# Kernel optimization log

Hardware: AMD Instinct MI355X
Metric: run time of the kernel (lower is better)

Reference implementation:

```python
import jax, jax.numpy as jnp
import numpy as np

B, C, H, W = 32, 512, 32, 32
N = H * W            # seq_len = 1024
HEADS = 8
DH = C // HEADS      # 64
K = 256              # linformer low-rank
EPS = 1e-5


def setup_inputs() -> dict:
    key = jax.random.key(0)
    ks = jax.random.split(key, 10)
    s = 0.02
    return {
        "x": jax.random.normal(ks[0], (B, C, H, W), dtype=jnp.float32),
        "pos": jax.random.normal(ks[1], (1, N, C), dtype=jnp.float32),
        "ln_g": jnp.ones((C,), dtype=jnp.float32),
        "ln_b": jnp.zeros((C,), dtype=jnp.float32),
        "Wq": jax.random.normal(ks[2], (C, C), dtype=jnp.float32) * s,
        "Wk": jax.random.normal(ks[3], (C, C), dtype=jnp.float32) * s,
        "Wv": jax.random.normal(ks[4], (C, C), dtype=jnp.float32) * s,
        "proj_k": jax.random.normal(ks[5], (N, K), dtype=jnp.float32) * s,
        "proj_v": jax.random.normal(ks[6], (N, K), dtype=jnp.float32) * s,
        "Wo": jax.random.normal(ks[7], (C, C), dtype=jnp.float32) * s,
        "bo": jnp.zeros((C,), dtype=jnp.float32),
    }


def reference(x, pos, ln_g, ln_b, Wq, Wk, Wv, proj_k, proj_v, Wo, bo):
    b, c, h, w = x.shape
    n = h * w
    # b c h w -> b (h w) c
    xf = x.reshape(b, c, n).transpose(0, 2, 1) + pos
    # LayerNorm (biased variance, eps=1e-5) + ReLU; dropout = identity (eval)
    mu = xf.mean(-1, keepdims=True)
    var = jnp.var(xf, axis=-1, keepdims=True)
    y = (xf - mu) * jax.lax.rsqrt(var + EPS) * ln_g + ln_b
    y = jax.nn.relu(y)
    # Linformer self-attention
    q = y @ Wq                                   # [b,n,c]
    k_ = jnp.einsum('bnd,nk->bkd', y @ Wk, proj_k)  # [b,K,c]
    v_ = jnp.einsum('bnd,nk->bkd', y @ Wv, proj_v)  # [b,K,c]
    q = q.reshape(b, n, HEADS, DH)
    k_ = k_.reshape(b, K, HEADS, DH)
    v_ = v_.reshape(b, K, HEADS, DH)
    dots = jnp.einsum('bnhd,bkhd->bhnk', q, k_) * (DH ** -0.5)
    attn = jax.nn.softmax(dots, axis=-1)
    out = jnp.einsum('bhnk,bkhd->bnhd', attn, v_).reshape(b, n, c)
    out = out @ Wo + bo
    # residual with (x + pos), then back to b c h w
    out = out + xf
    return out.transpose(0, 2, 1).reshape(b, c, h, w)
```

## Files before the change

### kernel.cpp

```cpp
#include <hip/hip_runtime.h>
#include <hip/hip_bf16.h>
#include <cstdint>

#define BB  32
#define CC  512
#define NN  1024
#define HH  8
#define DHH 64
#define KR  256

using f32x4  = __attribute__((ext_vector_type(4))) float;
using f32x16 = __attribute__((ext_vector_type(16))) float;
using bf16x8 = __attribute__((ext_vector_type(8))) __bf16;
using u32x4  = __attribute__((ext_vector_type(4))) unsigned int;

__device__ __forceinline__ unsigned short f2bf(float f) {
  unsigned int u = __float_as_uint(f);
  u += 0x7fffu + ((u >> 16) & 1u);
  return (unsigned short)(u >> 16);
}

__device__ __forceinline__ unsigned int pknat(float a, float b) {
  unsigned short ua = __builtin_bit_cast(unsigned short, (__bf16)a);
  unsigned short ub = __builtin_bit_cast(unsigned short, (__bf16)b);
  return (unsigned int)ua | ((unsigned int)ub << 16);
}

__device__ __forceinline__ void gload16(const void* gsrc, void* ldst) {
  __builtin_amdgcn_global_load_lds(
      (const __attribute__((address_space(1))) unsigned int*)gsrc,
      (__attribute__((address_space(3))) unsigned int*)ldst, 16, 0, 0);
}

__global__ __launch_bounds__(256) void transcvt_all(
    const float* __restrict__ w0, const float* __restrict__ w1,
    const float* __restrict__ w2, const float* __restrict__ w3,
    const float* __restrict__ p0, const float* __restrict__ p1,
    unsigned short* __restrict__ d0, unsigned short* __restrict__ d1,
    unsigned short* __restrict__ d2, unsigned short* __restrict__ d3,
    unsigned short* __restrict__ e0, unsigned short* __restrict__ e1) {
  const int m = blockIdx.y;
  const float* src = m==0?w0:m==1?w1:m==2?w2:m==3?w3:m==4?p0:p1;
  unsigned short* dst = m==0?d0:m==1?d1:m==2?d2:m==3?d3:m==4?e0:e1;
  const int R = (m < 4) ? 512 : 1024;
  const int logC = (m < 4) ? 9 : 8;
  int idx = blockIdx.x * 256 + threadIdx.x;
  int r = idx >> logC, c = idx & ((1 << logC) - 1);
  dst[(size_t)c * R + r] = f2bf(src[idx]);
}

__global__ __launch_bounds__(256) void posT_kernel(
    const float* __restrict__ pos, float* __restrict__ posT) {
  int idx = blockIdx.x * 256 + threadIdx.x;
  int c = idx >> 10, n = idx & 1023;
  posT[idx] = pos[(size_t)n * CC + c];
}

__global__ __launch_bounds__(256) void ln_relu_kernel(
    const float* __restrict__ x, const float* __restrict__ pos,
    const float* __restrict__ g, const float* __restrict__ bta,
    unsigned short* __restrict__ y, unsigned short* __restrict__ yT) {
  __shared__ float tile[16][528];
  __shared__ float smu[16], srs[16];
  const int b = blockIdx.y, n0 = blockIdx.x * 16;
  const int tid = threadIdx.x;
  const float* xb = x + (size_t)b * CC * NN;

  {
    const int q4 = (tid & 3) * 4;
    #pragma unroll
    for (int p = 0; p < 8; ++p) {
      int c = p * 64 + (tid >> 2);
      float4 v = *reinterpret_cast<const float4*>(&xb[(size_t)c * NN + n0 + q4]);
      tile[q4 + 0][c] = v.x;
      tile[q4 + 1][c] = v.y;
      tile[q4 + 2][c] = v.z;
      tile[q4 + 3][c] = v.w;
    }
  }
  __syncthreads();

  const int c4 = (tid & 127) * 4;
  #pragma unroll
  for (int p = 0; p < 8; ++p) {
    int nl = 2 * p + (tid >> 7);
    float4 pv = *reinterpret_cast<const float4*>(&pos[(size_t)(n0 + nl) * CC + c4]);
    float4* tp = reinterpret_cast<float4*>(&tile[nl][c4]);
    float4 t = *tp;
    t.x += pv.x; t.y += pv.y; t.z += pv.z; t.w += pv.w;
    *tp = t;
  }
  __syncthreads();

  {
    const int r = tid >> 4, l16 = tid & 15;
    float s = 0.f, s2 = 0.f;
    #pragma unroll
    for (int i = 0; i < 32; ++i) {
      float v = tile[r][l16 + i * 16];
      s += v; s2 += v * v;
    }
    #pragma unroll
    for (int d = 1; d < 16; d <<= 1) { s += __shfl_xor(s, d); s2 += __shfl_xor(s2, d); }
    if (l16 == 0) {
      float mu = s * (1.f / 512.f);
      float var = s2 * (1.f / 512.f) - mu * mu;
      smu[r] = mu;
      srs[r] = rsqrtf(var + 1e-5f);
    }
  }
  __syncthreads();

  unsigned short* yb = y + ((size_t)b * NN + n0) * CC;
  const float4 gv = *reinterpret_cast<const float4*>(&g[c4]);
  const float4 bv = *reinterpret_cast<const float4*>(&bta[c4]);
  #pragma unroll
  for (int p = 0; p < 8; ++p) {
    int nl = 2 * p + (tid >> 7);
    float mu = smu[nl], rs = srs[nl];
    float4* tp = reinterpret_cast<float4*>(&tile[nl][c4]);
    float4 t = *tp;
    float4 o;
    o.x = (t.x - mu) * rs * gv.x + bv.x; o.x = o.x > 0.f ? o.x : 0.f;
    o.y = (t.y - mu) * rs * gv.y + bv.y; o.y = o.y > 0.f ? o.y : 0.f;
    o.z = (t.z - mu) * rs * gv.z + bv.z; o.z = o.z > 0.f ? o.z : 0.f;
    o.w = (t.w - mu) * rs * gv.w + bv.w; o.w = o.w > 0.f ? o.w : 0.f;
    uint2 u; u.x = pknat(o.x, o.y); u.y = pknat(o.z, o.w);
    *reinterpret_cast<uint2*>(&yb[(size_t)nl * CC + c4]) = u;
    *tp = o;
  }
  __syncthreads();

  unsigned short* ytb = yT + (size_t)b * CC * NN + n0;
  #pragma unroll
  for (int h = 0; h < 2; ++h) {
    int cc = h * 256 + tid;
    unsigned int pk8[8];
    #pragma unroll
    for (int p = 0; p < 8; ++p)
      pk8[p] = pknat(tile[2 * p][cc], tile[2 * p + 1][cc]);
    *reinterpret_cast<uint4*>(&ytb[(size_t)cc * NN])     = *reinterpret_cast<uint4*>(&pk8[0]);
    *reinterpret_cast<uint4*>(&ytb[(size_t)cc * NN + 8]) = *reinterpret_cast<uint4*>(&pk8[4]);
  }
}

template <int MODE>
__global__ __launch_bounds__(256) void gemm_tn(
    const unsigned short* __restrict__ A, int lda, long long strideA,
    const unsigned short* __restrict__ Bt, int ldb, long long strideB,
    unsigned short* __restrict__ Cb, long long strideC,
    int Nn, int Kk, int TB,
    const float* __restrict__ xres, const float* __restrict__ posT,
    const float* __restrict__ bias, float* __restrict__ outF) {
  __shared__ __align__(16) unsigned short sh[17408];
  unsigned short* aL = sh;
  unsigned short* bL = sh + 8192;
  const int nb = blockIdx.x * 128, mb = blockIdx.y * 128, zb = blockIdx.z;
  A  += (size_t)strideA * zb;
  Bt += (size_t)strideB * zb;
  if (MODE == 0 || MODE == 1) Cb += (size_t)strideC * zb;
  const int tid  = threadIdx.x;
  const int lane = tid & 63;
  const int wave = tid >> 6;
  const int wm = (wave >> 1) * 64, wn = (wave & 1) * 64;
  const int sr  = lane >> 2;
  const int scw = lane & 3;
  f32x4 acc[4][4] = {};

  auto stage = [&](int buf, int k0) {
    #pragma unroll
    for (int i = 0; i < 2; ++i) {
      int rbase = wave * 32 + i * 16;
      int row = rbase + sr;
      int ca = scw ^ ((row ^ (row >> 2)) & 3);
      gload16(&A [(size_t)(mb + row) * lda + k0 + ca * 8], &aL[buf * 4096 + rbase * 32]);
      gload16(&Bt[(size_t)(nb + row) * ldb + k0 + ca * 8], &bL[buf * 4096 + rbase * 32]);
    }
  };

  const int nt = Kk >> 5;
  stage(0, 0);
  __syncthreads();

  for (int t = 0; t < nt; ++t) {
    const int buf = t & 1;
    if (t + 1 < nt) stage(buf ^ 1, (t + 1) << 5);

    bf16x8 af[4], bfv[4];
    const int kc = lane >> 4;
    #pragma unroll
    for (int i = 0; i < 4; ++i) {
      int ra = wm + i * 16 + (lane & 15);
      int rb = wn + i * 16 + (lane & 15);
      af[i]  = *reinterpret_cast<const bf16x8*>(&aL[buf * 4096 + ra * 32 + (kc ^ ((ra ^ (ra >> 2)) & 3)) * 8]);
      bfv[i] = *reinterpret_cast<const bf16x8*>(&bL[buf * 4096 + rb * 32 + (kc ^ ((rb ^ (rb >> 2)) & 3)) * 8]);
    }
    #pragma unroll
    for (int i = 0; i < 4; ++i)
      #pragma unroll
      for (int j = 0; j < 4; ++j)
        acc[i][j] = __builtin_amdgcn_mfma_f32_16x16x32_bf16(af[i], bfv[j], acc[i][j], 0, 0, 0);
    __syncthreads();
  }

  if (MODE == 2) {
    float* Ct = reinterpret_cast<float*>(sh);
    const int halfsel = wave >> 1;
    const int t0base = nb & 1023;
    const int bcell = nb >> 10;
    #pragma unroll
    for (int half = 0; half < 2; ++half) {
      __syncthreads();
      if (halfsel == half) {
        #pragma unroll
        for (int i = 0; i < 4; ++i) {
          int rloc = i * 16 + ((lane >> 4) << 2);
          #pragma unroll
          for (int j = 0; j < 4; ++j) {
            int cl = wn + j * 16 + (lane & 15);
            #pragma unroll
            for (int t = 0; t < 4; ++t)
              Ct[(rloc + t) * 132 + cl] = acc[i][j][t];
          }
        }
      }
      __syncthreads();
      #pragma unroll
      for (int p8 = 0; p8 < 8; ++p8) {
        int e = p8 * 256 + tid;
        int r = e >> 5, f4 = (e & 31) * 4;
        int c = mb + half * 64 + r;
        size_t base = ((size_t)bcell * CC + c) * NN + t0base + f4;
        float4 cv = *reinterpret_cast<const float4*>(&Ct[r * 132 + f4]);
        float4 xv = *reinterpret_cast<const float4*>(&xres[base]);
        float4 pv = *reinterpret_cast<const float4*>(&posT[(size_t)c * NN + t0base + f4]);
        float bc = bias[c];
        float4 ov;
        ov.x = cv.x + xv.x + pv.x + bc;
        ov.y = cv.y + xv.y + pv.y + bc;
        ov.z = cv.z + xv.z + pv.z + bc;
        ov.w = cv.w + xv.w + pv.w + bc;
        *reinterpret_cast<float4*>(&outF[base]) = ov;
      }
    }
  } else {
    auto Ct = (unsigned short (*)[136])sh;
    __syncthreads();
    #pragma unroll
    for (int i = 0; i < 4; ++i) {
      const int r0 = wm + i * 16 + ((lane >> 4) << 2);
      #pragma unroll
      for (int j = 0; j < 4; ++j) {
        const int cl = wn + j * 16 + (lane & 15);
        #pragma unroll
        for (int t = 0; t < 4; ++t) {
          if (MODE == 0) Ct[r0 + t][cl] = f2bf(acc[i][j][t]);
          else           Ct[cl][r0 + t] = f2bf(acc[i][j][t]);
        }
      }
    }
    __syncthreads();
    const int rr = tid >> 4, ch = tid & 15;
    #pragma unroll
    for (int it = 0; it < 8; ++it) {
      const int r = it * 16 + rr;
      uint4 v = *reinterpret_cast<const uint4*>(&Ct[r][ch * 8]);
      if (MODE == 0)
        *reinterpret_cast<uint4*>(&Cb[(size_t)(mb + r) * Nn + nb + ch * 8]) = v;
      else
        *reinterpret_cast<uint4*>(&Cb[(size_t)(nb + r) * TB + mb + ch * 8]) = v;
    }
  }
}

__global__ __launch_bounds__(256, 2) void attn_kernel(
    const unsigned short* __restrict__ q,
    const unsigned short* __restrict__ kB,
    const unsigned short* __restrict__ vT,
    unsigned short* __restrict__ O) {
  __shared__ __align__(16) unsigned short smem[32768];
  const int wgid = blockIdx.x;
  const int grp  = wgid & 255;
  const int tg   = wgid >> 8;
  const int h = grp & 7, b = grp >> 3;
  const int wave = threadIdx.x >> 6, lane = threadIdx.x & 63;
  const int t32 = lane & 31, g2 = lane >> 5;
  const int tokb = tg * 128 + wave * 32;

  const unsigned short* qp = q + ((size_t)(b * NN + tokb + t32)) * CC + h * DHH + g2 * 8;
  bf16x8 qf[4];
  #pragma unroll
  for (int st = 0; st < 4; ++st)
    qf[st] = *reinterpret_cast<const bf16x8*>(qp + (size_t)st * 16);

  {
    const unsigned short* kb = kB + ((size_t)b * KR) * CC + h * DHH;
    const int r0w = wave * 64;
    #pragma unroll
    for (int i = 0; i < 8; ++i) {
      int row = r0w + i * 8 + (lane >> 3);
      int sc  = (lane & 7) ^ (row & 7);
      gload16(kb + (size_t)row * CC + sc * 8, &smem[(r0w + i * 8) * 64]);
    }
    const unsigned short* vb = vT + ((size_t)b * CC + h * DHH) * KR;
    const int v0w = wave * 16;
    #pragma unroll
    for (int i = 0; i < 8; ++i) {
      int row = v0w + i * 2 + (lane >> 5);
      int sc  = (lane & 31) ^ (row & 7);
      gload16(vb + (size_t)row * KR + sc * 8, &smem[16384 + (v0w + i * 2) * 256]);
    }
  }
  __syncthreads();

  f32x16 s8[8] = {};
  #pragma unroll
  for (int t8 = 0; t8 < 8; ++t8) {
    const int row = t8 * 32 + t32;
    #pragma unroll
    for (int st = 0; st < 4; ++st) {
      int ch = (2 * st + g2) ^ (row & 7);
      bf16x8 kf = *reinterpret_cast<const bf16x8*>(&smem[row * 64 + ch * 8]);
      s8[t8] = __builtin_amdgcn_mfma_f32_32x32x16_bf16(kf, qf[st], s8[t8], 0, 0, 0);
    }
  }

  float m = -1e30f;
  #pragma unroll
  for (int t8 = 0; t8 < 8; ++t8)
    #pragma unroll
    for (int r = 0; r < 16; ++r) m = fmaxf(m, s8[t8][r]);
  m = fmaxf(m, __shfl_xor(m, 32));
  const float cexp = 0.125f * 1.44269504088896f;
  float ls = 0.f;
  #pragma unroll
  for (int t8 = 0; t8 < 8; ++t8)
    #pragma unroll
    for (int r = 0; r < 16; ++r) {
      float p = __builtin_amdgcn_exp2f((s8[t8][r] - m) * cexp);
      s8[t8][r] = p;
      ls += p;
    }
  ls += __shfl_xor(ls, 32);
  float rinv = __builtin_amdgcn_rcpf(ls);

  f32x16 o0 = {}, o1 = {};
  #pragma unroll
  for (int t8 = 0; t8 < 8; ++t8) {
    unsigned int pkd[8];
    #pragma unroll
    for (int qq = 0; qq < 4; ++qq) {
      pkd[qq * 2 + 0] = pknat(s8[t8][4 * qq + 0], s8[t8][4 * qq + 1]);
      pkd[qq * 2 + 1] = pknat(s8[t8][4 * qq + 2], s8[t8][4 * qq + 3]);
    }
    #pragma unroll
    for (int a = 0; a < 2; ++a) {
      const int ks = t8 * 2 + a;
      unsigned int xe0 = pkd[4 * a + 0], xe1 = pkd[4 * a + 1];
      unsigned int xo0 = pkd[4 * a + 2], xo1 = pkd[4 * a + 3];
      unsigned int d0 = g2 ? __shfl_xor(xo0, 32) : xe0;
      unsigned int d1 = g2 ? __shfl_xor(xo1, 32) : xe1;
      unsigned int d2 = g2 ? xo0 : __shfl_xor(xe0, 32);
      unsigned int d3 = g2 ? xo1 : __shfl_xor(xe1, 32);
      u32x4 pv_ = {d0, d1, d2, d3};
      bf16x8 pa = __builtin_bit_cast(bf16x8, pv_);
      #pragma unroll
      for (int dt = 0; dt < 2; ++dt) {
        int row = dt * 32 + t32;
        int ch = (2 * ks + g2) ^ (row & 7);
        bf16x8 bv = *reinterpret_cast<const bf16x8*>(&smem[16384 + row * 256 + ch * 8]);
        if (dt == 0) o0 = __builtin_amdgcn_mfma_f32_32x32x16_bf16(pa, bv, o0, 0, 0, 0);
        else         o1 = __builtin_amdgcn_mfma_f32_32x32x16_bf16(pa, bv, o1, 0, 0, 0);
      }
    }
  }

  unsigned short* Ob = O + ((size_t)(b * NN + tokb)) * CC + h * DHH;
  #pragma unroll
  for (int r = 0; r < 16; ++r) {
    int tl = (r & 3) + 8 * (r >> 2) + 4 * g2;
    float rs = __shfl(rinv, tl);
    Ob[(size_t)tl * CC + t32]      = f2bf(o0[r] * rs);
    Ob[(size_t)tl * CC + 32 + t32] = f2bf(o1[r] * rs);
  }
}

extern "C" void kernel_launch(void* const* d_in, const int* in_sizes, int n_in,
                              void* d_out, int out_size, void* d_ws, size_t ws_size,
                              hipStream_t stream) {
  const float* x    = (const float*)d_in[0];
  const float* pos  = (const float*)d_in[1];
  const float* ln_g = (const float*)d_in[2];
  const float* ln_b = (const float*)d_in[3];
  const float* Wq   = (const float*)d_in[4];
  const float* Wk   = (const float*)d_in[5];
  const float* Wv   = (const float*)d_in[6];
  const float* pk   = (const float*)d_in[7];
  const float* pv   = (const float*)d_in[8];
  const float* Wo   = (const float*)d_in[9];
  const float* bo   = (const float*)d_in[10];
  float* out = (float*)d_out;

  unsigned short* ws = (unsigned short*)d_ws;
  size_t off = 0;
  auto alloc = [&](size_t elems) { unsigned short* p = ws + off; off += elems; return p; };
  unsigned short* WqT     = alloc(512 * 512);
  unsigned short* WkT     = alloc(512 * 512);
  unsigned short* WvT     = alloc(512 * 512);
  unsigned short* WoT     = alloc(512 * 512);
  unsigned short* projcat = alloc((size_t)512 * 1024);
  float*          posTb   = (float*)alloc((size_t)512 * 1024 * 2);
  unsigned short* yB      = alloc((size_t)32768 * 512);
  unsigned short* yT      = alloc((size_t)32 * 512 * 1024);
  unsigned short* qB      = alloc((size_t)32768 * 512);
  unsigned short* zB      = alloc((size_t)32 * 512 * 512);
  unsigned short* kBuf    = alloc((size_t)32 * 256 * 512);
  unsigned short* vTB     = alloc((size_t)32 * 512 * 256);
  unsigned short* OB      = alloc((size_t)32768 * 512);

  transcvt_all<<<dim3(1024, 6), 256, 0, stream>>>(
      Wq, Wk, Wv, Wo, pk, pv,
      WqT, WkT, WvT, WoT, projcat, projcat + (size_t)256 * 1024);
  posT_kernel<<<2048, 256, 0, stream>>>(pos, posTb);

  ln_relu_kernel<<<dim3(64, 32), 256, 0, stream>>>(x, pos, ln_g, ln_b, yB, yT);

  gemm_tn<0><<<dim3(4, 256), 256, 0, stream>>>(
      yB, 512, 0, WqT, 512, 0, qB, 0, 512, 512, 0, nullptr, nullptr, nullptr, nullptr);

  gemm_tn<0><<<dim3(4, 4, 32), 256, 0, stream>>>(
      projcat, 1024, 0, yT, 1024, (long long)512 * 1024, zB, (long long)512 * 512,
      512, 1024, 0, nullptr, nullptr, nullptr, nullptr);

  gemm_tn<0><<<dim3(4, 2, 32), 256, 0, stream>>>(
      zB, 512, (long long)512 * 512, WkT, 512, 0, kBuf, (long long)256 * 512,
      512, 512, 0, nullptr, nullptr, nullptr, nullptr);

  gemm_tn<1><<<dim3(4, 2, 32), 256, 0, stream>>>(
      zB + (size_t)256 * 512, 512, (long long)512 * 512, WvT, 512, 0,
      vTB, (long long)512 * 256, 512, 512, 256, nullptr, nullptr, nullptr, nullptr);

  attn_kernel<<<dim3(2048, 1, 1), 256, 0, stream>>>(qB, kBuf, vTB, OB);

  gemm_tn<2><<<dim3(256, 4), 256, 0, stream>>>(
      WoT, 512, 0, OB, 512, 0, nullptr, 0, 32768, 512, 0, x, posTb, bo, out);
}
```

Measured before the change: 220.3 us.

## Triple-buffer GEMM loads, merge K/V projection GEMMs, prefetch pos in LayerNorm

The bf16 GEMM moves from double to triple buffering in LDS. It stages two K-tiles ahead and uses explicit vmcnt waits with a raw s_barrier instead of __syncthreads each iteration, so global loads overlap more MFMA work. The two separate K and V projection GEMMs become a single launch through a new MODE 3, which picks the weight matrix and output layout per blockIdx.y. This assumes WvT sits directly after WkT in memory. The LayerNorm kernel issues its pos loads into registers before the transpose phase and shrinks the tile row padding; the extra LDS and register use may lower occupancy.

```diff
diff --git a/kernel.cpp b/kernel.cpp
--- a/kernel.cpp
+++ b/kernel.cpp
@@ -60,11 +60,19 @@
     const float* __restrict__ x, const float* __restrict__ pos,
     const float* __restrict__ g, const float* __restrict__ bta,
     unsigned short* __restrict__ y, unsigned short* __restrict__ yT) {
-  __shared__ float tile[16][528];
+  __shared__ float tile[16][516];
   __shared__ float smu[16], srs[16];
   const int b = blockIdx.y, n0 = blockIdx.x * 16;
   const int tid = threadIdx.x;
   const float* xb = x + (size_t)b * CC * NN;
+  const int c4 = (tid & 127) * 4;
+
+  float4 pr[8];
+  #pragma unroll
+  for (int p = 0; p < 8; ++p) {
+    int nl = 2 * p + (tid >> 7);
+    pr[p] = *reinterpret_cast<const float4*>(&pos[(size_t)(n0 + nl) * CC + c4]);
+  }
 
   {
     const int q4 = (tid & 3) * 4;
@@ -80,14 +88,12 @@
   }
   __syncthreads();
 
-  const int c4 = (tid & 127) * 4;
   #pragma unroll
   for (int p = 0; p < 8; ++p) {
     int nl = 2 * p + (tid >> 7);
-    float4 pv = *reinterpret_cast<const float4*>(&pos[(size_t)(n0 + nl) * CC + c4]);
     float4* tp = reinterpret_cast<float4*>(&tile[nl][c4]);
     float4 t = *tp;
-    t.x += pv.x; t.y += pv.y; t.z += pv.z; t.w += pv.w;
+    t.x += pr[p].x; t.y += pr[p].y; t.z += pr[p].z; t.w += pr[p].w;
     *tp = t;
   }
   __syncthreads();
@@ -149,16 +155,27 @@
     const unsigned short* __restrict__ A, int lda, long long strideA,
     const unsigned short* __restrict__ Bt, int ldb, long long strideB,
     unsigned short* __restrict__ Cb, long long strideC,
+    unsigned short* __restrict__ Cb2, long long strideC2,
     int Nn, int Kk, int TB,
     const float* __restrict__ xres, const float* __restrict__ posT,
     const float* __restrict__ bias, float* __restrict__ outF) {
-  __shared__ __align__(16) unsigned short sh[17408];
+  __shared__ __align__(16) unsigned short sh[24576];
   unsigned short* aL = sh;
-  unsigned short* bL = sh + 8192;
-  const int nb = blockIdx.x * 128, mb = blockIdx.y * 128, zb = blockIdx.z;
+  unsigned short* bL = sh + 12288;
+  const int zb = blockIdx.z;
+  int sel = 0, mb;
+  if (MODE == 3) {
+    sel = blockIdx.y >> 1;
+    mb = ((blockIdx.y & 1) + sel * 2) * 128;
+    if (sel == 1) Bt += (size_t)512 * 512;
+  } else {
+    mb = blockIdx.y * 128;
+  }
+  const int nb = blockIdx.x * 128;
   A  += (size_t)strideA * zb;
   Bt += (size_t)strideB * zb;
-  if (MODE == 0 || MODE == 1) Cb += (size_t)strideC * zb;
+  Cb += (size_t)strideC * zb;
+  if (MODE == 3) Cb2 += (size_t)strideC2 * zb;
   const int tid  = threadIdx.x;
   const int lane = tid & 63;
   const int wave = tid >> 6;
@@ -180,11 +197,14 @@
 
   const int nt = Kk >> 5;
   stage(0, 0);
-  __syncthreads();
-
+  stage(1, 32);
+  asm volatile("s_waitcnt vmcnt(4)" ::: "memory");
+  __builtin_amdgcn_s_barrier();
+  __builtin_amdgcn_sched_barrier(0);
+
+  int cbuf = 0;
   for (int t = 0; t < nt; ++t) {
-    const int buf = t & 1;
-    if (t + 1 < nt) stage(buf ^ 1, (t + 1) << 5);
+    if (t + 2 < nt) stage(cbuf == 0 ? 2 : cbuf - 1, (t + 2) << 5);
 
     bf16x8 af[4], bfv[4];
     const int kc = lane >> 4;
@@ -192,15 +212,22 @@
     for (int i = 0; i < 4; ++i) {
       int ra = wm + i * 16 + (lane & 15);
       int rb = wn + i * 16 + (lane & 15);
-      af[i]  = *reinterpret_cast<const bf16x8*>(&aL[buf * 4096 + ra * 32 + (kc ^ ((ra ^ (ra >> 2)) & 3)) * 8]);
-      bfv[i] = *reinterpret_cast<const bf16x8*>(&bL[buf * 4096 + rb * 32 + (kc ^ ((rb ^ (rb >> 2)) & 3)) * 8]);
+      af[i]  = *reinterpret_cast<const bf16x8*>(&aL[cbuf * 4096 + ra * 32 + (kc ^ ((ra ^ (ra >> 2)) & 3)) * 8]);
+      bfv[i] = *reinterpret_cast<const bf16x8*>(&bL[cbuf * 4096 + rb * 32 + (kc ^ ((rb ^ (rb >> 2)) & 3)) * 8]);
     }
     #pragma unroll
     for (int i = 0; i < 4; ++i)
       #pragma unroll
       for (int j = 0; j < 4; ++j)
         acc[i][j] = __builtin_amdgcn_mfma_f32_16x16x32_bf16(af[i], bfv[j], acc[i][j], 0, 0, 0);
-    __syncthreads();
+
+    if (t + 2 < nt)      { asm volatile("s_waitcnt vmcnt(4)" ::: "memory"); }
+    else if (t + 1 < nt) { asm volatile("s_waitcnt vmcnt(0)" ::: "memory"); }
+    if (t + 1 < nt) {
+      __builtin_amdgcn_s_barrier();
+      __builtin_amdgcn_sched_barrier(0);
+    }
+    cbuf = (cbuf == 2) ? 0 : cbuf + 1;
   }
 
   if (MODE == 2) {
@@ -244,6 +271,7 @@
       }
     }
   } else {
+    const bool transp = (MODE == 1) || (MODE == 3 && sel == 1);
     auto Ct = (unsigned short (*)[136])sh;
     __syncthreads();
     #pragma unroll
@@ -254,8 +282,8 @@
         const int cl = wn + j * 16 + (lane & 15);
         #pragma unroll
         for (int t = 0; t < 4; ++t) {
-          if (MODE == 0) Ct[r0 + t][cl] = f2bf(acc[i][j][t]);
-          else           Ct[cl][r0 + t] = f2bf(acc[i][j][t]);
+          if (!transp) Ct[r0 + t][cl] = f2bf(acc[i][j][t]);
+          else         Ct[cl][r0 + t] = f2bf(acc[i][j][t]);
         }
       }
     }
@@ -265,10 +293,12 @@
     for (int it = 0; it < 8; ++it) {
       const int r = it * 16 + rr;
       uint4 v = *reinterpret_cast<const uint4*>(&Ct[r][ch * 8]);
-      if (MODE == 0)
+      if (!transp)
         *reinterpret_cast<uint4*>(&Cb[(size_t)(mb + r) * Nn + nb + ch * 8]) = v;
+      else if (MODE == 1)
+        *reinterpret_cast<uint4*>(&Cb[(size_t)(nb + r) * TB + mb + ch * 8]) = v;
       else
-        *reinterpret_cast<uint4*>(&Cb[(size_t)(nb + r) * TB + mb + ch * 8]) = v;
+        *reinterpret_cast<uint4*>(&Cb2[(size_t)(nb + r) * TB + (mb - 256) + ch * 8]) = v;
     }
   }
 }
@@ -426,22 +456,20 @@
   ln_relu_kernel<<<dim3(64, 32), 256, 0, stream>>>(x, pos, ln_g, ln_b, yB, yT);
 
   gemm_tn<0><<<dim3(4, 256), 256, 0, stream>>>(
-      yB, 512, 0, WqT, 512, 0, qB, 0, 512, 512, 0, nullptr, nullptr, nullptr, nullptr);
+      yB, 512, 0, WqT, 512, 0, qB, 0, nullptr, 0,
+      512, 512, 0, nullptr, nullptr, nullptr, nullptr);
 
   gemm_tn<0><<<dim3(4, 4, 32), 256, 0, stream>>>(
       projcat, 1024, 0, yT, 1024, (long long)512 * 1024, zB, (long long)512 * 512,
-      512, 1024, 0, nullptr, nullptr, nullptr, nullptr);
-
-  gemm_tn<0><<<dim3(4, 2, 32), 256, 0, stream>>>(
+      nullptr, 0, 512, 1024, 0, nullptr, nullptr, nullptr, nullptr);
+
+  gemm_tn<3><<<dim3(4, 4, 32), 256, 0, stream>>>(
       zB, 512, (long long)512 * 512, WkT, 512, 0, kBuf, (long long)256 * 512,
-      512, 512, 0, nullptr, nullptr, nullptr, nullptr);
-
-  gemm_tn<1><<<dim3(4, 2, 32), 256, 0, stream>>>(
-      zB + (size_t)256 * 512, 512, (long long)512 * 512, WvT, 512, 0,
       vTB, (long long)512 * 256, 512, 512, 256, nullptr, nullptr, nullptr, nullptr);
 
   attn_kernel<<<dim3(2048, 1, 1), 256, 0, stream>>>(qB, kBuf, vTB, OB);
 
   gemm_tn<2><<<dim3(256, 4), 256, 0, stream>>>(
-      WoT, 512, 0, OB, 512, 0, nullptr, 0, 32768, 512, 0, x, posTb, bo, out);
-}
+      WoT, 512, 0, OB, 512, 0, nullptr, 0, nullptr, 0,
+      32768, 512, 0, x, posTb, bo, out);
+}
```

Measured after the change: 212.1 us. 3.7% less time.
